# Kernel tuning notes

Measured on AMD Instinct MI355X. Metric: run time of the kernel, lower is better.

## Reference

```python
import jax, jax.numpy as jnp
import numpy as np

N = 100000   # nodes
E = 1000000  # edges
D = 128      # in_dim == out_dim (residual enabled)
EPS = 1e-5   # BatchNorm1d default eps


def setup_inputs() -> dict:
    key = jax.random.key(0)
    k = jax.random.split(key, 5)
    feature = jax.random.normal(k[0], (N, D), dtype=jnp.float32)
    src = jax.random.randint(k[1], (E,), 0, N, dtype=jnp.int32)
    dst = jax.random.randint(k[2], (E,), 0, N, dtype=jnp.int32)
    # nn.Linear(in_dim, out_dim): W is [out, in]
    W = jax.random.normal(k[3], (D, D), dtype=jnp.float32) / np.sqrt(D).astype(np.float32)
    b = jnp.zeros((D,), dtype=jnp.float32)
    gamma = jnp.ones((D,), dtype=jnp.float32)
    beta = jnp.zeros((D,), dtype=jnp.float32)
    return {"feature": feature, "src": src, "dst": dst, "W": W, "b": b,
            "gamma": gamma, "beta": beta}


def reference(feature, src, dst, W, b, gamma, beta):
    # update_all(copy_src('h'), mean): gather src features, mean-reduce onto dst
    deg = jax.ops.segment_sum(jnp.ones((E,), dtype=feature.dtype), dst,
                              num_segments=N)                      # [N]
    agg = jax.ops.segment_sum(feature[src], dst, num_segments=N)   # [N, D]
    agg = agg / jnp.maximum(deg, 1.0)[:, None]  # zero in-degree -> 0 (DGL mean)
    # NodeApplyModule: linear
    h = agg @ W.T + b                                              # [N, D]
    # BatchNorm1d over node dimension (training-mode batch stats, biased var)
    mean = jnp.mean(h, axis=0)
    var = jnp.var(h, axis=0)
    h = (h - mean) * jax.lax.rsqrt(var + EPS) * gamma + beta
    # activation, residual; dropout p=0.0 -> identity
    h = jax.nn.relu(h)
    h = feature + h
    return h
```

## Files before the change

kernel.cpp:

```cpp
#include <hip/hip_runtime.h>

typedef unsigned short u16;
typedef unsigned int u32;

#define D_DIM 128
#define CHUNK 4096
#define SCHUNK 4096
#define NPART 8

typedef __attribute__((ext_vector_type(8))) short bf16x8;
typedef __attribute__((ext_vector_type(4))) float f32x4;

__device__ __forceinline__ float bf2f(u16 h) {
    u32 u = ((u32)h) << 16;
    return __uint_as_float(u);
}
__device__ __forceinline__ u16 f2bf(float f) {
    u32 u = __float_as_uint(f);
    u32 r = (u >> 16) & 1u;
    u += 0x7fffu + r;
    return (u16)(u >> 16);
}
__device__ __forceinline__ float lo16(u32 u) { return bf2f((u16)(u & 0xffffu)); }
__device__ __forceinline__ float hi16(u32 u) { return bf2f((u16)(u >> 16)); }

__global__ void GCNLayer_76647986365164_kernel(
        int* p, int nwords, const u32* w, int* flag,
        const float* __restrict__ f, u16* __restrict__ fb,
        const void* __restrict__ W, u16* __restrict__ wpre,
        int total8, int zb) {
    const int tid = threadIdx.x;
    const int b = blockIdx.x;
    if (b < zb) {
        int i = b * 256 + tid;
        if (i < nwords) p[i] = 0;
        return;
    }
    __shared__ int cnt;
    if (tid == 0) cnt = 0;
    __syncthreads();
    {
        int c = 0;
        for (int j = 0; j < 4; ++j) {
            u32 x = w[tid * 4 + j];
            u32 e = (x >> 7) & 0xFFu;
            if (e >= 100u && e <= 140u) c++;
        }
        atomicAdd(&cnt, c);
    }
    __syncthreads();
    const int bf = (cnt >= 700) ? 1 : 0;
    if (b == zb && tid == 0) flag[0] = bf;

    if (b == gridDim.x - 1) {
        #pragma unroll
        for (int i = 0; i < 8; ++i) {
            int idx = i * 256 + tid;
            int frag = idx >> 6, dl = idx & 63;
            int ot = frag >> 2, kt = frag & 3;
            int dg = dl >> 4, dc = dl & 15;
            int row = ot * 16 + dc, col = kt * 32 + dg * 8;
            if (bf) {
                *(uint4*)(wpre + (size_t)idx * 8) =
                    *(const uint4*)((const u16*)W + row * 128 + col);
            } else {
                const float* Wf = (const float*)W;
                float4 x = *(const float4*)(Wf + row * 128 + col);
                float4 y = *(const float4*)(Wf + row * 128 + col + 4);
                float v[8] = {x.x, x.y, x.z, x.w, y.x, y.y, y.z, y.w};
                u16 h0[8], h1[8];
                #pragma unroll
                for (int j = 0; j < 8; ++j) {
                    h0[j] = f2bf(v[j]);
                    h1[j] = f2bf(v[j] - bf2f(h0[j]));
                }
                uint4 p0, p1;
                p0.x = (u32)h0[0] | ((u32)h0[1] << 16);
                p0.y = (u32)h0[2] | ((u32)h0[3] << 16);
                p0.z = (u32)h0[4] | ((u32)h0[5] << 16);
                p0.w = (u32)h0[6] | ((u32)h0[7] << 16);
                p1.x = (u32)h1[0] | ((u32)h1[1] << 16);
                p1.y = (u32)h1[2] | ((u32)h1[3] << 16);
                p1.z = (u32)h1[4] | ((u32)h1[5] << 16);
                p1.w = (u32)h1[6] | ((u32)h1[7] << 16);
                *(uint4*)(wpre + (size_t)idx * 8) = p0;
                *(uint4*)(wpre + 16384 + (size_t)idx * 8) = p1;
            }
        }
        return;
    }
    if (bf) return;
    int i = (b - zb) * 256 + tid;
    if (i >= total8) return;
    float4 a = ((const float4*)f)[i * 2];
    float4 bb = ((const float4*)f)[i * 2 + 1];
    uint4 o;
    o.x = (u32)f2bf(a.x) | ((u32)f2bf(a.y) << 16);
    o.y = (u32)f2bf(a.z) | ((u32)f2bf(a.w) << 16);
    o.z = (u32)f2bf(bb.x) | ((u32)f2bf(bb.y) << 16);
    o.w = (u32)f2bf(bb.z) | ((u32)f2bf(bb.w) << 16);
    ((uint4*)fb)[i] = o;
}

__global__ void k_deg(const int* __restrict__ dst, int* __restrict__ deg,
                      int* __restrict__ rank, int E) {
    int i = (blockIdx.x * blockDim.x + threadIdx.x) * 4;
    if (i + 3 < E) {
        int4 d = *(const int4*)(dst + i);
        int4 r;
        r.x = atomicAdd(&deg[d.x], 1);
        r.y = atomicAdd(&deg[d.y], 1);
        r.z = atomicAdd(&deg[d.z], 1);
        r.w = atomicAdd(&deg[d.w], 1);
        *(int4*)(rank + i) = r;
    } else {
        for (; i < E; ++i) rank[i] = atomicAdd(&deg[dst[i]], 1);
    }
}

__global__ void k_scan_local(const int* deg, int* offs, int* bsums, int n) {
    __shared__ int tsum[256];
    const int tid = threadIdx.x;
    const int base = blockIdx.x * CHUNK + tid * 16;
    int v[16];
    int run = 0;
    for (int j = 0; j < 16; ++j) {
        int idx = base + j;
        v[j] = (idx < n) ? deg[idx] : 0;
        run += v[j];
    }
    tsum[tid] = run;
    __syncthreads();
    for (int off = 1; off < 256; off <<= 1) {
        int val = tsum[tid];
        int add = (tid >= off) ? tsum[tid - off] : 0;
        __syncthreads();
        tsum[tid] = val + add;
        __syncthreads();
    }
    int acc = tsum[tid] - run;
    for (int j = 0; j < 16; ++j) {
        int idx = base + j;
        if (idx < n) offs[idx] = acc;
        acc += v[j];
    }
    if (tid == 255) bsums[blockIdx.x] = tsum[255];
}

__global__ void k_scan_add(int* offs, const int* bsums, int n, int nblk) {
    __shared__ int carry_s;
    const int tid = threadIdx.x;
    const int b = blockIdx.x;
    if (tid == 0) {
        int c = 0;
        for (int i = 0; i < b; ++i) c += bsums[i];
        carry_s = c;
        if (b == nblk - 1) offs[n] = c + bsums[b];
    }
    __syncthreads();
    const int carry = carry_s;
    const int base = b * CHUNK + tid * 16;
    for (int j = 0; j < 16; ++j) {
        int idx = base + j;
        if (idx < n) offs[idx] += carry;
    }
}

__global__ void k_scatter(const int* __restrict__ src, const int* __restrict__ dst,
                          const int* __restrict__ rank, const int* __restrict__ offs,
                          int* __restrict__ csr, int E, int nper) {
    const int pr = blockIdx.x & (NPART - 1);
    const int s  = blockIdx.x >> 3;
    const int lo = pr * nper;
    const int hi = lo + nper;
    const int base = s * SCHUNK;
    int end = base + SCHUNK;
    if (end > E) end = E;
    for (int i = base + (int)threadIdx.x; i < end; i += 256) {
        int d = dst[i];
        if (d >= lo && d < hi) {
            csr[offs[d] + rank[i]] = src[i];
        }
    }
}

__global__ void k_aggregate(const void* feature, const u16* __restrict__ fcopy,
                            const int* offs, const int* csr, u16* agg,
                            const int* flag, int n, int npad) {
    const int tid = threadIdx.x;
    const int node = blockIdx.x * 16 + (tid >> 4);
    const int c = tid & 15;
    if (node >= npad) return;
    const u16* fb = flag[0] ? (const u16*)feature : fcopy;
    const uint4* fq = (const uint4*)fb;
    float acc[8];
    #pragma unroll
    for (int t = 0; t < 8; ++t) acc[t] = 0.f;
    int degn = 0;
    if (node < n) {
        int s = offs[node], e = offs[node + 1];
        degn = e - s;
        for (int j = s; j < e; j += 4) {
            int j1 = j + 1, j2 = j + 2, j3 = j + 3;
            uint4 u0 = {0,0,0,0}, u1 = {0,0,0,0}, u2 = {0,0,0,0}, u3 = {0,0,0,0};
            u0 = fq[(size_t)csr[j] * 16 + c];
            if (j1 < e) u1 = fq[(size_t)csr[j1] * 16 + c];
            if (j2 < e) u2 = fq[(size_t)csr[j2] * 16 + c];
            if (j3 < e) u3 = fq[(size_t)csr[j3] * 16 + c];
            #define ACC8(U) \
                acc[0] += lo16(U.x); acc[1] += hi16(U.x); \
                acc[2] += lo16(U.y); acc[3] += hi16(U.y); \
                acc[4] += lo16(U.z); acc[5] += hi16(U.z); \
                acc[6] += lo16(U.w); acc[7] += hi16(U.w);
            ACC8(u0); ACC8(u1); ACC8(u2); ACC8(u3);
            #undef ACC8
        }
    }
    float sc = 1.0f / (float)(degn > 1 ? degn : 1);
    uint4 o4;
    o4.x = (u32)f2bf(acc[0] * sc) | ((u32)f2bf(acc[1] * sc) << 16);
    o4.y = (u32)f2bf(acc[2] * sc) | ((u32)f2bf(acc[3] * sc) << 16);
    o4.z = (u32)f2bf(acc[4] * sc) | ((u32)f2bf(acc[5] * sc) << 16);
    o4.w = (u32)f2bf(acc[6] * sc) | ((u32)f2bf(acc[7] * sc) << 16);
    ((uint4*)(agg + (size_t)node * D_DIM))[c] = o4;
}

__global__ __launch_bounds__(512, 4)
void k_gemm(u16* __restrict__ agg, const u16* __restrict__ wpre,
            const void* __restrict__ bias, float* __restrict__ parts,
            const int* __restrict__ flag, int n) {
    __shared__ u16 sW[2048 * 8];
    const int tid = threadIdx.x;
    const int rb = blockIdx.x * 128;
    const int bf = flag[0];
    const int w = tid >> 6;
    const int lane = tid & 63;
    const int g = lane >> 4, c = lane & 15;

    bf16x8 afr[4];
    {
        const u16* arow = agg + (size_t)(rb + w * 16 + c) * D_DIM + g * 8;
        #pragma unroll
        for (int kt = 0; kt < 4; ++kt)
            afr[kt] = *(const bf16x8*)(arow + kt * 32);
    }

    f32x4 acc[8];
    #pragma unroll
    for (int ot = 0; ot < 8; ++ot) acc[ot] = (f32x4){0.f, 0.f, 0.f, 0.f};

    const int npass = bf ? 1 : 2;
    for (int pass = 0; pass < npass; ++pass) {
        if (pass) __syncthreads();
        const u16* wsrc = wpre + (size_t)pass * 16384;
        #pragma unroll
        for (int i = 0; i < 4; ++i) {
            int idx = i * 512 + tid;
            *(uint4*)(&sW[idx * 8]) = *(const uint4*)(wsrc + (size_t)idx * 8);
        }
        __syncthreads();
        #pragma unroll
        for (int ot = 0; ot < 8; ++ot) {
            #pragma unroll
            for (int kt = 0; kt < 4; ++kt) {
                bf16x8 bfr = *(const bf16x8*)(&sW[((ot * 4 + kt) * 64 + lane) * 8]);
                acc[ot] = __builtin_amdgcn_mfma_f32_16x16x32_bf16(
                    afr[kt], bfr, acc[ot], 0, 0, 0);
            }
        }
    }

    float* red = (float*)sW;
    __syncthreads();

    const int rowbase = rb + w * 16 + g * 4;
    #pragma unroll
    for (int ot = 0; ot < 8; ++ot) {
        const int o = ot * 16 + c;
        float bv = bf ? bf2f(((const u16*)bias)[o]) : ((const float*)bias)[o];
        float s = 0.f, q = 0.f;
        float hv[4];
        #pragma unroll
        for (int r = 0; r < 4; ++r) {
            float h = acc[ot][r] + bv;
            hv[r] = h;
            if (rowbase + r < n) { s += h; q += h * h; }
        }
        #pragma unroll
        for (int r = 0; r < 4; ++r) {
            float hp = __shfl_xor(hv[r], 1);
            if (!(lane & 1)) {
                u32 pk = (u32)f2bf(hv[r]) | ((u32)f2bf(hp) << 16);
                *(u32*)(agg + (size_t)(rowbase + r) * D_DIM + o) = pk;
            }
        }
        s += __shfl_xor(s, 16); s += __shfl_xor(s, 32);
        q += __shfl_xor(q, 16); q += __shfl_xor(q, 32);
        if (g == 0) { red[w * 256 + o] = s; red[w * 256 + 128 + o] = q; }
    }
    __syncthreads();
    if (tid < 256) {
        float a = 0.f;
        #pragma unroll
        for (int ww = 0; ww < 8; ++ww) a += red[ww * 256 + tid];
        parts[(size_t)blockIdx.x * 256 + tid] = a;
    }
}

__global__ void k_redstats(const float* __restrict__ partials,
                           float* __restrict__ stats, int nb) {
    const int tid = threadIdx.x;
    float a0 = 0.f, a1 = 0.f, a2 = 0.f, a3 = 0.f;
    float a4 = 0.f, a5 = 0.f, a6 = 0.f, a7 = 0.f;
    for (int r0 = blockIdx.x * 8; r0 < nb; r0 += gridDim.x * 8) {
        if (r0 + 0 < nb) a0 += partials[(size_t)(r0 + 0) * 256 + tid];
        if (r0 + 1 < nb) a1 += partials[(size_t)(r0 + 1) * 256 + tid];
        if (r0 + 2 < nb) a2 += partials[(size_t)(r0 + 2) * 256 + tid];
        if (r0 + 3 < nb) a3 += partials[(size_t)(r0 + 3) * 256 + tid];
        if (r0 + 4 < nb) a4 += partials[(size_t)(r0 + 4) * 256 + tid];
        if (r0 + 5 < nb) a5 += partials[(size_t)(r0 + 5) * 256 + tid];
        if (r0 + 6 < nb) a6 += partials[(size_t)(r0 + 6) * 256 + tid];
        if (r0 + 7 < nb) a7 += partials[(size_t)(r0 + 7) * 256 + tid];
    }
    float s = ((a0 + a1) + (a2 + a3)) + ((a4 + a5) + (a6 + a7));
    atomicAdd(&stats[tid], s);
}

__global__ void k_apply(const u16* h, const void* feature, const float* stats,
                        const void* gamma, const void* beta, void* outp,
                        const int* flag, int total8, float invn) {
    __shared__ float ssc[128], ssh[128];
    int tid = threadIdx.x;
    int bf = flag[0];
    if (tid < 128) {
        float mean = stats[tid] * invn;
        float var = stats[128 + tid] * invn - mean * mean;
        var = fmaxf(var, 0.f);
        float inv = rsqrtf(var + 1e-5f);
        float g = bf ? bf2f(((const u16*)gamma)[tid]) : ((const float*)gamma)[tid];
        float bb = bf ? bf2f(((const u16*)beta)[tid]) : ((const float*)beta)[tid];
        float sc = inv * g;
        ssc[tid] = sc;
        ssh[tid] = bb - mean * sc;
    }
    __syncthreads();
    int i = blockIdx.x * 256 + tid;
    if (i >= total8) return;
    size_t base = (size_t)i * 8;
    int c0 = (int)(base & (D_DIM - 1));
    uint4 h4 = ((const uint4*)h)[i];
    u32 hw[4] = {h4.x, h4.y, h4.z, h4.w};
    float hv[8];
    for (int j = 0; j < 4; ++j) { hv[2*j] = lo16(hw[j]); hv[2*j+1] = hi16(hw[j]); }
    float fv[8];
    if (bf) {
        uint4 f4 = ((const uint4*)feature)[i];
        u32 fw[4] = {f4.x, f4.y, f4.z, f4.w};
        for (int j = 0; j < 4; ++j) { fv[2*j] = lo16(fw[j]); fv[2*j+1] = hi16(fw[j]); }
    } else {
        float4 fa = ((const float4*)feature)[i * 2];
        float4 fb = ((const float4*)feature)[i * 2 + 1];
        fv[0]=fa.x; fv[1]=fa.y; fv[2]=fa.z; fv[3]=fa.w;
        fv[4]=fb.x; fv[5]=fb.y; fv[6]=fb.z; fv[7]=fb.w;
    }
    float ov[8];
    for (int j = 0; j < 8; ++j)
        ov[j] = fmaxf(hv[j] * ssc[c0 + j] + ssh[c0 + j], 0.f) + fv[j];
    if (bf) {
        uint4 o4;
        u32 ow[4];
        for (int j = 0; j < 4; ++j)
            ow[j] = (u32)f2bf(ov[2*j]) | ((u32)f2bf(ov[2*j+1]) << 16);
        o4.x = ow[0]; o4.y = ow[1]; o4.z = ow[2]; o4.w = ow[3];
        ((uint4*)outp)[i] = o4;
    } else {
        float4 oa, ob;
        oa.x=ov[0]; oa.y=ov[1]; oa.z=ov[2]; oa.w=ov[3];
        ob.x=ov[4]; ob.y=ov[5]; ob.z=ov[6]; ob.w=ov[7];
        ((float4*)outp)[i * 2] = oa;
        ((float4*)outp)[i * 2 + 1] = ob;
    }
}

static inline size_t al256s(size_t x) { return (x + 255) & ~(size_t)255; }
static inline int gmax1(int x) { return x > 0 ? x : 1; }

extern "C" void kernel_launch(void* const* d_in, const int* in_sizes, int n_in,
                              void* d_out, int out_size, void* d_ws, size_t ws_size,
                              hipStream_t stream) {
    const void* feature = d_in[0];
    const int*  src     = (const int*)d_in[1];
    const int*  dst     = (const int*)d_in[2];
    const void* W       = d_in[3];
    const void* bias    = d_in[4];
    const void* gamma   = d_in[5];
    const void* beta    = d_in[6];

    const int N = in_sizes[0] / D_DIM;
    const int E = in_sizes[1];
    const int Npad = (N + 127) & ~127;
    const int nblk = (N + CHUNK - 1) / CHUNK;
    const int nper = (N + NPART - 1) / NPART;
    const int gb   = Npad / 128;

    char* p = (char*)d_ws;
    size_t o = 0;
    int*   flag   = (int*)(p + o);      o += 256;
    int*   deg    = (int*)(p + o);      o += (size_t)N * 4;
    float* stats  = (float*)(p + o);    o += 256 * 4;
    const int zero_words = N + 256;
    o = al256s(o);
    u16*   wpre   = (u16*)(p + o);      o += al256s(2 * 16384 * 2);
    int*   bsums  = (int*)(p + o);      o += al256s(((size_t)nblk + 8) * 4);
    int*   offs   = (int*)(p + o);      o += al256s(((size_t)N + 8) * 4);
    int*   csr    = (int*)(p + o);      o += al256s((size_t)E * 4);
    float* parts  = (float*)(p + o);    o += al256s((size_t)gb * 256 * 4);
    u16*   agg    = (u16*)(p + o);      o += al256s((size_t)Npad * D_DIM * 2);
    int*   rank   = (int*)agg;
    u16*   fbf    = (u16*)d_out;
    (void)ws_size; (void)n_in; (void)out_size;

    int total8 = N * D_DIM / 8;
    int zb = gmax1((zero_words + 255) / 256);
    int tb = gmax1((total8 + 255) / 256);
    int sblocks = gmax1(((E + SCHUNK - 1) / SCHUNK) * NPART);

    GCNLayer_76647986365164_kernel<<<zb + tb + 1, 256, 0, stream>>>(
        deg, zero_words, (const u32*)feature, flag,
        (const float*)feature, fbf, W, wpre, total8, zb);
    k_deg<<<gmax1((E + 1023) / 1024), 256, 0, stream>>>(dst, deg, rank, E);
    k_scan_local<<<gmax1(nblk), 256, 0, stream>>>(deg, offs, bsums, N);
    k_scan_add<<<gmax1(nblk), 256, 0, stream>>>(offs, bsums, N, nblk);
    k_scatter<<<sblocks, 256, 0, stream>>>(src, dst, rank, offs, csr, E, nper);
    k_aggregate<<<gmax1(Npad / 16), 256, 0, stream>>>(
        feature, fbf, offs, csr, agg, flag, N, Npad);
    k_gemm<<<gmax1(gb), 512, 0, stream>>>(agg, wpre, bias, parts, flag, N);
    k_redstats<<<32, 256, 0, stream>>>(parts, stats, gb);
    k_apply<<<gmax1((total8 + 255) / 256), 256, 0, stream>>>(
        agg, feature, stats, gamma, beta, d_out, flag, total8, 1.0f / (float)N);
}
```

Baseline: 290.2 us.

## Build CSR with LDS-privatized striped histograms instead of global atomics

Replaces the global-atomic degree count plus per-edge rank array with a two-pass counting sort. Edges are split into 32 stripes and nodes into partitions, and each block histograms its partition in shared memory. A column scan then turns the per-stripe counts into bases, and the scatter pass recomputes local ranks with shared-memory atomics. The carry step in k_scan_add now uses a wave-parallel shuffle reduction instead of a single-thread loop. This removes the contended global atomics, at the cost of reading dst several times (once per partition) and storing a 32×N count matrix. Within a stripe, edge order in the CSR is no longer deterministic.

```diff
diff --git a/kernel.cpp b/kernel.cpp
--- a/kernel.cpp
+++ b/kernel.cpp
@@ -5,8 +5,8 @@
 
 #define D_DIM 128
 #define CHUNK 4096
-#define SCHUNK 4096
-#define NPART 8
+#define NSTRIPE 32
+#define LCN 12800
 
 typedef __attribute__((ext_vector_type(8))) short bf16x8;
 typedef __attribute__((ext_vector_type(4))) float f32x4;
@@ -102,20 +102,53 @@
     ((uint4*)fb)[i] = o;
 }
 
-__global__ void k_deg(const int* __restrict__ dst, int* __restrict__ deg,
-                      int* __restrict__ rank, int E) {
-    int i = (blockIdx.x * blockDim.x + threadIdx.x) * 4;
-    if (i + 3 < E) {
-        int4 d = *(const int4*)(dst + i);
-        int4 r;
-        r.x = atomicAdd(&deg[d.x], 1);
-        r.y = atomicAdd(&deg[d.y], 1);
-        r.z = atomicAdd(&deg[d.z], 1);
-        r.w = atomicAdd(&deg[d.w], 1);
-        *(int4*)(rank + i) = r;
-    } else {
-        for (; i < E; ++i) rank[i] = atomicAdd(&deg[dst[i]], 1);
-    }
+__global__ __launch_bounds__(256)
+void k_hist(const int* __restrict__ dst, int* __restrict__ cnt,
+            int E, int N, int nper, int ES, int P) {
+    __shared__ int lc[LCN];
+    const int tid = threadIdx.x;
+    const int p = blockIdx.x % P;
+    const int s = blockIdx.x / P;
+    const int lo = p * nper;
+    const int hi = min(lo + nper, N);
+    const int cn = hi - lo;
+    for (int t = tid; t < cn; t += 256) lc[t] = 0;
+    __syncthreads();
+    const int base = s * ES;
+    const int end = min(base + ES, E);
+    for (int i = base + tid * 4; i < end; i += 1024) {
+        if (i + 3 < end) {
+            int4 d4 = *(const int4*)(dst + i);
+            if (d4.x >= lo && d4.x < hi) atomicAdd(&lc[d4.x - lo], 1);
+            if (d4.y >= lo && d4.y < hi) atomicAdd(&lc[d4.y - lo], 1);
+            if (d4.z >= lo && d4.z < hi) atomicAdd(&lc[d4.z - lo], 1);
+            if (d4.w >= lo && d4.w < hi) atomicAdd(&lc[d4.w - lo], 1);
+        } else {
+            for (int k = i; k < end; ++k) {
+                int d = dst[k];
+                if (d >= lo && d < hi) atomicAdd(&lc[d - lo], 1);
+            }
+        }
+    }
+    __syncthreads();
+    int* crow = cnt + (size_t)s * N + lo;
+    for (int t = tid; t < cn; t += 256) crow[t] = lc[t];
+}
+
+__global__ void k_colscan(int* __restrict__ cnt, int* __restrict__ deg, int N) {
+    int n = blockIdx.x * 256 + threadIdx.x;
+    if (n >= N) return;
+    int c[NSTRIPE];
+    #pragma unroll
+    for (int s = 0; s < NSTRIPE; ++s) c[s] = cnt[(size_t)s * N + n];
+    int run = 0;
+    #pragma unroll
+    for (int s = 0; s < NSTRIPE; ++s) {
+        int t = c[s];
+        cnt[(size_t)s * N + n] = run;
+        run += t;
+    }
+    deg[n] = run;
 }
 
 __global__ void k_scan_local(const int* deg, int* offs, int* bsums, int n) {
@@ -151,11 +184,15 @@
     __shared__ int carry_s;
     const int tid = threadIdx.x;
     const int b = blockIdx.x;
-    if (tid == 0) {
-        int c = 0;
-        for (int i = 0; i < b; ++i) c += bsums[i];
-        carry_s = c;
-        if (b == nblk - 1) offs[n] = c + bsums[b];
+    if (tid < 64) {
+        int acc = 0;
+        for (int k = tid; k < b; k += 64) acc += bsums[k];
+        #pragma unroll
+        for (int off = 1; off < 64; off <<= 1) acc += __shfl_xor(acc, off);
+        if (tid == 0) {
+            carry_s = acc;
+            if (b == nblk - 1) offs[n] = acc + bsums[b];
+        }
     }
     __syncthreads();
     const int carry = carry_s;
@@ -166,20 +203,50 @@
     }
 }
 
-__global__ void k_scatter(const int* __restrict__ src, const int* __restrict__ dst,
-                          const int* __restrict__ rank, const int* __restrict__ offs,
-                          int* __restrict__ csr, int E, int nper) {
-    const int pr = blockIdx.x & (NPART - 1);
-    const int s  = blockIdx.x >> 3;
-    const int lo = pr * nper;
-    const int hi = lo + nper;
-    const int base = s * SCHUNK;
-    int end = base + SCHUNK;
-    if (end > E) end = E;
-    for (int i = base + (int)threadIdx.x; i < end; i += 256) {
-        int d = dst[i];
-        if (d >= lo && d < hi) {
-            csr[offs[d] + rank[i]] = src[i];
+__global__ __launch_bounds__(256)
+void k_scatter(const int* __restrict__ src, const int* __restrict__ dst,
+               const int* __restrict__ bases, const int* __restrict__ offs,
+               int* __restrict__ csr, int E, int N, int nper, int ES, int P) {
+    __shared__ int lc[LCN];
+    const int tid = threadIdx.x;
+    const int p = blockIdx.x % P;
+    const int s = blockIdx.x / P;
+    const int lo = p * nper;
+    const int hi = min(lo + nper, N);
+    const int cn = hi - lo;
+    for (int t = tid; t < cn; t += 256) lc[t] = 0;
+    __syncthreads();
+    const int base = s * ES;
+    const int end = min(base + ES, E);
+    const int* brow = bases + (size_t)s * N;
+    for (int i = base + tid * 4; i < end; i += 1024) {
+        if (i + 3 < end) {
+            int4 d4 = *(const int4*)(dst + i);
+            int4 s4 = *(const int4*)(src + i);
+            if (d4.x >= lo && d4.x < hi) {
+                int lr = atomicAdd(&lc[d4.x - lo], 1);
+                csr[offs[d4.x] + brow[d4.x] + lr] = s4.x;
+            }
+            if (d4.y >= lo && d4.y < hi) {
+                int lr = atomicAdd(&lc[d4.y - lo], 1);
+                csr[offs[d4.y] + brow[d4.y] + lr] = s4.y;
+            }
+            if (d4.z >= lo && d4.z < hi) {
+                int lr = atomicAdd(&lc[d4.z - lo], 1);
+                csr[offs[d4.z] + brow[d4.z] + lr] = s4.z;
+            }
+            if (d4.w >= lo && d4.w < hi) {
+                int lr = atomicAdd(&lc[d4.w - lo], 1);
+                csr[offs[d4.w] + brow[d4.w] + lr] = s4.w;
+            }
+        } else {
+            for (int k = i; k < end; ++k) {
+                int d = dst[k];
+                if (d >= lo && d < hi) {
+                    int lr = atomicAdd(&lc[d - lo], 1);
+                    csr[offs[d] + brow[d] + lr] = src[k];
+                }
+            }
         }
     }
 }
@@ -400,15 +467,17 @@
     const int E = in_sizes[1];
     const int Npad = (N + 127) & ~127;
     const int nblk = (N + CHUNK - 1) / CHUNK;
-    const int nper = (N + NPART - 1) / NPART;
     const int gb   = Npad / 128;
+
+    int P = (N + LCN - 1) / LCN;  if (P < 8) P = 8;
+    const int nper = (N + P - 1) / P;
+    const int ES = (((E + NSTRIPE - 1) / NSTRIPE) + 3) & ~3;
 
     char* p = (char*)d_ws;
     size_t o = 0;
     int*   flag   = (int*)(p + o);      o += 256;
-    int*   deg    = (int*)(p + o);      o += (size_t)N * 4;
+    int*   deg    = (int*)(p + o);      o += al256s((size_t)N * 4);
     float* stats  = (float*)(p + o);    o += 256 * 4;
-    const int zero_words = N + 256;
     o = al256s(o);
     u16*   wpre   = (u16*)(p + o);      o += al256s(2 * 16384 * 2);
     int*   bsums  = (int*)(p + o);      o += al256s(((size_t)nblk + 8) * 4);
@@ -416,22 +485,24 @@
     int*   csr    = (int*)(p + o);      o += al256s((size_t)E * 4);
     float* parts  = (float*)(p + o);    o += al256s((size_t)gb * 256 * 4);
     u16*   agg    = (u16*)(p + o);      o += al256s((size_t)Npad * D_DIM * 2);
-    int*   rank   = (int*)agg;
+    int*   cnt    = (int*)agg;
     u16*   fbf    = (u16*)d_out;
     (void)ws_size; (void)n_in; (void)out_size;
 
     int total8 = N * D_DIM / 8;
-    int zb = gmax1((zero_words + 255) / 256);
+    int zb = 1;
     int tb = gmax1((total8 + 255) / 256);
-    int sblocks = gmax1(((E + SCHUNK - 1) / SCHUNK) * NPART);
+    int hblocks = NSTRIPE * P;
 
     GCNLayer_76647986365164_kernel<<<zb + tb + 1, 256, 0, stream>>>(
-        deg, zero_words, (const u32*)feature, flag,
+        (int*)stats, 256, (const u32*)feature, flag,
         (const float*)feature, fbf, W, wpre, total8, zb);
-    k_deg<<<gmax1((E + 1023) / 1024), 256, 0, stream>>>(dst, deg, rank, E);
+    k_hist<<<hblocks, 256, 0, stream>>>(dst, cnt, E, N, nper, ES, P);
+    k_colscan<<<gmax1((N + 255) / 256), 256, 0, stream>>>(cnt, deg, N);
     k_scan_local<<<gmax1(nblk), 256, 0, stream>>>(deg, offs, bsums, N);
     k_scan_add<<<gmax1(nblk), 256, 0, stream>>>(offs, bsums, N, nblk);
-    k_scatter<<<sblocks, 256, 0, stream>>>(src, dst, rank, offs, csr, E, nper);
+    k_scatter<<<hblocks, 256, 0, stream>>>(src, dst, cnt, offs, csr,
+                                           E, N, nper, ES, P);
     k_aggregate<<<gmax1(Npad / 16), 256, 0, stream>>>(
         feature, fbf, offs, csr, agg, flag, N, Npad);
     k_gemm<<<gmax1(gb), 512, 0, stream>>>(agg, wpre, bias, parts, flag, N);
```

New measurement: 319.5 us. 1.1x slower.
